# Kernel tuning notes

Hardware: AMD Instinct MI355X
Metric: run time of the kernel (lower is better)

Reference implementation:

```python
import jax, jax.numpy as jnp
import numpy as np

NNK = 16
DENSITY_WEIGHT = 1.0


def _sq_dist(x, y):
    # x: [B, Nx, C], y: [B, Ny, C] -> [B, Nx, Ny] squared L2 distances.
    # Matmul form of the original broadcast-diff computation (same math,
    # avoids materializing [B, Nx, C, Ny]); clamp tiny negatives from fp error.
    x2 = jnp.sum(x * x, axis=-1)               # [B, Nx]
    y2 = jnp.sum(y * y, axis=-1)               # [B, Ny]
    xy = jnp.einsum('bnc,bmc->bnm', x, y)      # [B, Nx, Ny]
    return jnp.maximum(x2[:, :, None] + y2[:, None, :] - 2.0 * xy, 0.0)


def _safe_sqrt(s):
    # sqrt with zero (instead of inf) gradient at s == 0; forward values exact.
    pos = s > 0
    return jnp.where(pos, jnp.sqrt(jnp.where(pos, s, 1.0)), 0.0)


def setup_inputs() -> dict:
    key = jax.random.key(0)
    k1, k2 = jax.random.split(key)
    B, N, C = 2, 8192, 3
    y_pred = jax.random.normal(k1, (B, N, C), dtype=jnp.float32)
    y_true = jax.random.normal(k2, (B, N, C), dtype=jnp.float32)
    return {"y_pred": y_pred, "y_true": y_true}


def reference(y_pred, y_true):
    # dist[b, i, j] = || y_true[b, i] - y_pred[b, j] ||
    dist = _safe_sqrt(_sq_dist(y_true, y_pred))            # [B, Nt, Np]
    minrow = jnp.min(dist, axis=2)                         # per true point
    mincol = jnp.min(dist, axis=1)                         # per pred point
    shape_loss = (jnp.mean(minrow) + jnp.mean(mincol)) / 2

    dist2 = _safe_sqrt(_sq_dist(y_true, y_true))           # [B, Nt, Nt]
    knndis, _ = jax.lax.top_k(-dist, NNK)                  # [B, Nt, k]
    knndis2, _ = jax.lax.top_k(-dist2, NNK)                # [B, Nt, k]
    density_loss = jnp.mean(jnp.abs(knndis - knndis2))

    data_loss = shape_loss + density_loss * DENSITY_WEIGHT
    return (data_loss, shape_loss, density_loss)
```

## Files before the change

kernel.cpp:

```cpp
#include <hip/hip_runtime.h>
#include <math.h>

#define NPTS 8192
#define NB 2
#define NROWS (NB * NPTS)
#define KNN 16
#define KC 6

#define GRID 32
#define NCELLS (GRID * GRID * GRID)
#define TOTCELLS (4 * NCELLS)
#define H 0.35f
#define RLO (-5.6f)
#define INVH (1.0f / H)
#define SCAN_BLOCKS 128
#define SEGCAP 132

__device__ __forceinline__ int cellof(float x) {
  int c = (int)floorf((x - RLO) * INVH);
  return min(max(c, 0), GRID - 1);
}

__device__ __forceinline__ float sqd3(float qx, float qy, float qz, float4 c) {
  float dx = qx - c.x, dy = qy - c.y, dz = qz - c.z;
  return fmaf(dx, dx, fmaf(dy, dy, dz * dz));
}

__device__ __forceinline__ int lanerank(unsigned long long mk) {
  return __builtin_amdgcn_mbcnt_hi((unsigned)(mk >> 32),
                                   __builtin_amdgcn_mbcnt_lo((unsigned)mk, 0));
}

template <int K>
__device__ __forceinline__ void insertK(float (&a)[K], float d) {
  if (d < a[K - 1]) {
    a[K - 1] = d;
#pragma unroll
    for (int k = K - 1; k > 0; --k) {
      float lo = fminf(a[k - 1], a[k]);
      a[k] = fmaxf(a[k - 1], a[k]);
      a[k - 1] = lo;
    }
  }
}

__device__ __forceinline__ float bitonic_sort64(float v, int lane) {
#pragma unroll
  for (int k = 2; k <= 64; k <<= 1) {
#pragma unroll
    for (int j = k >> 1; j >= 1; j >>= 1) {
      float o = __shfl_xor(v, j, 64);
      bool up = ((lane & k) == 0);
      bool lower = ((lane & j) == 0);
      float mn = fminf(v, o), mx = fmaxf(v, o);
      v = (up == lower) ? mn : mx;
    }
  }
  return v;
}

template <int K, int NEED>
__device__ void wave_grid_knn(int g, float qx, float qy, float qz,
                              const float4* __restrict__ sorted,
                              const unsigned* __restrict__ pack,
                              unsigned* sS, unsigned* sC, unsigned* sPre,
                              int lane, float (&a)[K], float& dmin,
                              int& cnt, float& bnd2) {
  const int cx = cellof(qx), cy = cellof(qy), cz = cellof(qz);
  float fx = fminf(qx - (RLO + cx * H), (RLO + (cx + 1) * H) - qx);
  float fy = fminf(qy - (RLO + cy * H), (RLO + (cy + 1) * H) - qy);
  float fz = fminf(qz - (RLO + cz * H), (RLO + (cz + 1) * H) - qz);
  const float fq = fminf(fx, fminf(fy, fz));
  const int base = g * NCELLS;
  for (int m = 0; m <= GRID; ++m) {
    const int zlo = max(cz - m, 0), zhi = min(cz + m, GRID - 1);
    const int ylo = max(cy - m, 0), yhi = min(cy + m, GRID - 1);
    const int xlo = max(cx - m, 0), xhi = min(cx + m, GRID - 1);
    const int ny = yhi - ylo + 1;
    const int nrows = (zhi - zlo + 1) * ny;
    for (int rb = 0; rb < nrows; rb += 64) {
      const int rho = rb + lane;
      const bool act = rho < nrows;
      const int rr = act ? rho : 0;
      const int z = zlo + rr / ny, y = ylo + rr % ny;
      const int dza = abs(z - cz), dya = abs(y - cy);
      const bool bdry = (dza == m) || (dya == m);
      unsigned stA = 0, cnA = 0, stB = 0, cnB = 0;
      const int rowbase = base + (z * GRID + y) * GRID;
      if (act) {
        if (bdry) {
          unsigned plo = pack[rowbase + xlo];
          unsigned phi = pack[rowbase + xhi];
          stA = plo >> 14;
          cnA = ((phi >> 14) + (phi & 16383u)) - stA;
        } else {
          int xl = cx - m, xr = cx + m;
          if (xl >= 0) { unsigned p = pack[rowbase + xl]; stA = p >> 14; cnA = p & 16383u; }
          if (xr < GRID) { unsigned p = pack[rowbase + xr]; stB = p >> 14; cnB = p & 16383u; }
        }
      }
      unsigned long long mA = __ballot(cnA > 0);
      unsigned long long mB = __ballot(cnB > 0);
      int nA = __popcll(mA);
      int nseg = nA + __popcll(mB);
      if (nseg == 0) continue;
      int slA = lanerank(mA), slB = nA + lanerank(mB);
      if (cnA > 0) { sS[slA] = stA; sC[slA] = cnA; }
      if (cnB > 0) { sS[slB] = stB; sC[slB] = cnB; }
      unsigned total = 0;
      for (int h = 0; h < 2; ++h) {
        int sl = h * 64 + lane;
        unsigned v = (sl < nseg) ? sC[sl] : 0u;
        unsigned inc = v;
#pragma unroll
        for (int s2 = 1; s2 < 64; s2 <<= 1) {
          unsigned t = __shfl_up(inc, s2, 64);
          if (lane >= s2) inc += t;
        }
        if (sl < nseg) sPre[sl] = total + inc - v;
        total += __shfl(inc, 63, 64);
        if (nseg <= 64) break;
      }
      int sh0 = (nseg > 1) ? (1 << (31 - __clz(nseg - 1))) : 0;
      for (unsigned cb = 0; cb < total; cb += 64) {
        unsigned c = cb + (unsigned)lane;
        bool cact = c < total;
        unsigned cc = cact ? c : (total - 1);
        int lo = 0;
        for (int sh = sh0; sh; sh >>= 1) {
          int mid = lo + sh;
          if (mid < nseg && sPre[mid] <= cc) lo = mid;
        }
        float4 p = sorted[sS[lo] + (cc - sPre[lo])];
        float d = cact ? sqd3(qx, qy, qz, p) : INFINITY;
        dmin = fminf(dmin, fmaxf(d, a[K - 1]));
        insertK(a, d);
      }
    }
    float bnd = fmaxf((float)m * H + fq, 0.0f) * 0.999f;
    bnd2 = bnd * bnd;
    int c = 0;
#pragma unroll
    for (int k = 0; k < K; ++k) c += (a[k] <= bnd2) ? 1 : 0;
#pragma unroll
    for (int s2 = 1; s2 < 64; s2 <<= 1) c += __shfl_xor(c, s2, 64);
    cnt = c;
    bool covered = (zlo == 0 && zhi == GRID - 1 && ylo == 0 && yhi == GRID - 1 &&
                    xlo == 0 && xhi == GRID - 1);
    if (c >= NEED || covered) break;
  }
}

__global__ __launch_bounds__(256) void count_kernel(
    const float* __restrict__ yp, const float* __restrict__ yt,
    unsigned* __restrict__ counts, int* __restrict__ pflat,
    unsigned* __restrict__ prank) {
  int t = blockIdx.x * 256 + threadIdx.x;
  const float* src;
  int g;
  if (t < NROWS) { src = yp + 3 * t; g = 2 * (t >> 13); }
  else { int u = t - NROWS; src = yt + 3 * u; g = 2 * (u >> 13) + 1; }
  int flat = g * NCELLS + (cellof(src[2]) * GRID + cellof(src[1])) * GRID + cellof(src[0]);
  unsigned r = atomicAdd(&counts[flat], 1u);
  pflat[t] = flat;
  prank[t] = r;
}

__global__ __launch_bounds__(1024) void scan1_kernel(
    const unsigned* __restrict__ counts, unsigned* __restrict__ partial,
    unsigned* __restrict__ aux) {
  __shared__ unsigned s[1024];
  int t = threadIdx.x;
  int base = blockIdx.x * 1024;
  unsigned v = counts[base + t];
  s[t] = v;
  __syncthreads();
  for (int off = 1; off < 1024; off <<= 1) {
    unsigned add = (t >= off) ? s[t - off] : 0u;
    __syncthreads();
    s[t] += add;
    __syncthreads();
  }
  partial[base + t] = s[t] - v;
  if (t == 1023) aux[blockIdx.x] = s[t];
}

__global__ __launch_bounds__(1024) void pack_kernel(
    const unsigned* __restrict__ counts, const unsigned* __restrict__ partial,
    const unsigned* __restrict__ aux, unsigned* __restrict__ pack) {
  __shared__ unsigned sa[2];
  const int t = threadIdx.x;
  if (t < 128) {
    unsigned v = (t < (int)blockIdx.x) ? aux[t] : 0u;
#pragma unroll
    for (int s = 1; s < 64; s <<= 1) v += __shfl_xor(v, s, 64);
    if ((t & 63) == 0) sa[t >> 6] = v;
  }
  __syncthreads();
  unsigned base = sa[0] + sa[1];
  int i = blockIdx.x * 1024 + t;
  pack[i] = ((partial[i] + base) << 14) | counts[i];
}

__global__ __launch_bounds__(256) void scatter_kernel(
    const float* __restrict__ yp, const float* __restrict__ yt,
    const unsigned* __restrict__ pack, const int* __restrict__ pflat,
    const unsigned* __restrict__ prank, float4* __restrict__ sorted) {
  int t = blockIdx.x * 256 + threadIdx.x;
  const float* src;
  int row;
  if (t < NROWS) { row = t; src = yp + 3 * t; }
  else { row = t - NROWS; src = yt + 3 * row; }
  unsigned pos = (pack[pflat[t]] >> 14) + prank[t];
  sorted[pos] = make_float4(src[0], src[1], src[2], __int_as_float(row));
}

__global__ __launch_bounds__(256) void query_kernel(
    const float4* __restrict__ sorted, const unsigned* __restrict__ pack,
    float* __restrict__ knnP, float* __restrict__ knnT,
    float* __restrict__ mincol_arr, unsigned* __restrict__ flags) {
  __shared__ unsigned sb[4][3][SEGCAP];
  __shared__ float cbw[4][64];
  const int wave = threadIdx.x >> 6, lane = threadIdx.x & 63;
  const int wid = blockIdx.x * 4 + wave;
  const int type = wid >> 14;
  const int qid = wid & 16383;
  const int b = qid >> 13;
  const int src_g = (type == 2) ? 2 * b : 2 * b + 1;
  const int tgt_g = (type == 0) ? 2 * b : 2 * b + 1;
  float4 e = sorted[src_g * NPTS + (qid & (NPTS - 1))];
  const int row = __float_as_int(e.w);
  unsigned* sS = sb[wave][0];
  unsigned* sC = sb[wave][1];
  unsigned* sP = sb[wave][2];
  float* cbuf = cbw[wave];
  if (type < 2) {
    float a[KC];
#pragma unroll
    for (int k = 0; k < KC; ++k) a[k] = INFINITY;
    float dmin = INFINITY, bnd2;
    int cnt;
    wave_grid_knn<KC, KNN>(tgt_g, e.x, e.y, e.z, sorted, pack, sS, sC, sP,
                           lane, a, dmin, cnt, bnd2);
    float tau;
    if (cnt >= KNN && cnt <= 64) {
      tau = bnd2;
    } else {
      float slm = bitonic_sort64(a[0], lane);
      tau = __shfl(slm, 15, 64);
    }
    int tot = 0;
    int idx[KC];
#pragma unroll
    for (int k = 0; k < KC; ++k) {
      unsigned long long mk = __ballot(a[k] <= tau);
      idx[k] = tot + lanerank(mk);
      tot += __popcll(mk);
    }
#pragma unroll
    for (int k = 0; k < KC; ++k)
      if (a[k] <= tau && idx[k] < 64) cbuf[idx[k]] = a[k];
    float v = (lane < tot) ? cbuf[lane] : INFINITY;
    v = bitonic_sort64(v, lane);
    float f15 = __shfl(v, 15, 64);
    bool bad = (tot > 64) || (__ballot(dmin <= f15) != 0ull);
    float* dst = (type == 0) ? knnP : knnT;
    if (lane < KNN) dst[row * KNN + lane] = sqrtf(v);
    if (lane == 0) flags[type * NROWS + row] = bad ? 1u : 0u;
  } else {
    float a1[1] = {INFINITY};
    float dmin = INFINITY, bnd2;
    int cnt;
    wave_grid_knn<1, 1>(tgt_g, e.x, e.y, e.z, sorted, pack, sS, sC, sP,
                        lane, a1, dmin, cnt, bnd2);
    float v = a1[0];
#pragma unroll
    for (int s = 1; s < 64; s <<= 1) v = fminf(v, __shfl_xor(v, s, 64));
    if (lane == 0) mincol_arr[row] = sqrtf(v);
  }
}

__device__ float exact16_rowlist(const float4* __restrict__ base,
                                 float qx, float qy, float qz, int lane) {
  float a[KNN];
#pragma unroll
  for (int k = 0; k < KNN; ++k) a[k] = INFINITY;
  for (int s = 0; s < NPTS / 64; ++s) {
    float d = sqd3(qx, qy, qz, base[s * 64 + lane]);
    insertK(a, d);
  }
  float res = INFINITY;
#pragma unroll 1
  for (int r = 0; r < KNN; ++r) {
    float v = a[0];
    int idx = lane;
#pragma unroll
    for (int s = 1; s < 64; s <<= 1) {
      float ov = __shfl_xor(v, s, 64);
      int oi = __shfl_xor(idx, s, 64);
      bool take = (ov < v) || (ov == v && oi < idx);
      v = take ? ov : v;
      idx = take ? oi : idx;
    }
    if (lane == r) res = v;
    if (lane == idx) {
#pragma unroll
      for (int k = 0; k < KNN - 1; ++k) a[k] = a[k + 1];
      a[KNN - 1] = INFINITY;
    }
  }
  return res;
}

__global__ __launch_bounds__(256) void combine_kernel(
    const float* __restrict__ yt, const float4* __restrict__ sorted,
    const unsigned* __restrict__ flags, float* __restrict__ knnP,
    float* __restrict__ knnT, const float* __restrict__ mincol_arr,
    double* __restrict__ pd) {
  __shared__ double s1[256], s2[256], s3[256];
  const int t = threadIdx.x, lane = t & 63, wave = t >> 6;
  const int row0 = blockIdx.x * 256;
  const int rbase = row0 + wave * 64;
  unsigned f0 = flags[rbase + lane];
  unsigned f1 = flags[NROWS + rbase + lane];
  unsigned long long m0 = __ballot(f0 != 0u);
  unsigned long long m1 = __ballot(f1 != 0u);
  while (m0) {
    int rr = __ffsll(m0) - 1; m0 &= m0 - 1;
    int row = rbase + rr;
    int bb = row >> 13;
    const float* q = yt + 3 * row;
    float s = exact16_rowlist(sorted + (size_t)(2 * bb) * NPTS, q[0], q[1], q[2], lane);
    if (lane < KNN) knnP[row * KNN + lane] = sqrtf(s);
  }
  while (m1) {
    int rr = __ffsll(m1) - 1; m1 &= m1 - 1;
    int row = rbase + rr;
    int bb = row >> 13;
    const float* q = yt + 3 * row;
    float s = exact16_rowlist(sorted + (size_t)(2 * bb + 1) * NPTS, q[0], q[1], q[2], lane);
    if (lane < KNN) knnT[row * KNN + lane] = sqrtf(s);
  }
  __syncthreads();
  const int row = row0 + t;
  float s = 0.0f;
#pragma unroll
  for (int k = 0; k < KNN; ++k)
    s += fabsf(knnP[row * KNN + k] - knnT[row * KNN + k]);
  s1[t] = (double)knnP[row * KNN];
  s2[t] = (double)mincol_arr[row];
  s3[t] = (double)s;
  __syncthreads();
  for (int off = 128; off > 0; off >>= 1) {
    if (t < off) { s1[t] += s1[t + off]; s2[t] += s2[t + off]; s3[t] += s3[t + off]; }
    __syncthreads();
  }
  if (t == 0) {
    pd[blockIdx.x * 3 + 0] = s1[0];
    pd[blockIdx.x * 3 + 1] = s2[0];
    pd[blockIdx.x * 3 + 2] = s3[0];
  }
}

__global__ __launch_bounds__(64) void finalize_kernel(
    const double* __restrict__ pd, float* __restrict__ out) {
  const int t = threadIdx.x;
  double a = pd[t * 3], b = pd[t * 3 + 1], c = pd[t * 3 + 2];
#pragma unroll
  for (int s = 32; s >= 1; s >>= 1) {
    a += __shfl_down(a, s, 64);
    b += __shfl_down(b, s, 64);
    c += __shfl_down(c, s, 64);
  }
  if (t == 0) {
    double shape = 0.5 * (a + b) / (double)NROWS;
    double dens = c / ((double)NROWS * KNN);
    out[0] = (float)(shape + dens);
    out[1] = (float)shape;
    out[2] = (float)dens;
  }
}

extern "C" void kernel_launch(void* const* d_in, const int* in_sizes, int n_in,
                              void* d_out, int out_size, void* d_ws, size_t ws_size,
                              hipStream_t stream) {
  (void)in_sizes; (void)n_in; (void)out_size; (void)ws_size;
  const float* yp = (const float*)d_in[0];
  const float* yt = (const float*)d_in[1];
  char* w = (char*)d_ws;
  unsigned* counts  = (unsigned*)w;  w += TOTCELLS * 4;
  unsigned* partial = (unsigned*)w;  w += TOTCELLS * 4;
  unsigned* aux     = (unsigned*)w;  w += 512;
  unsigned* pack    = (unsigned*)w;  w += TOTCELLS * 4;
  int*      pflat   = (int*)w;       w += 2 * NROWS * 4;
  unsigned* prank   = (unsigned*)w;  w += 2 * NROWS * 4;
  float4*   sorted  = (float4*)w;    w += 2 * NROWS * 16;
  float*    knnP    = (float*)w;     w += NROWS * KNN * 4;
  float*    knnT    = (float*)w;     w += NROWS * KNN * 4;
  float*    mincol  = (float*)w;     w += NROWS * 4;
  unsigned* flags   = (unsigned*)w;  w += 2 * NROWS * 4;
  double*   pd      = (double*)w;    w += 64 * 3 * 8;
  float* out = (float*)d_out;

  hipMemsetAsync(counts, 0, (size_t)TOTCELLS * 4, stream);
  count_kernel<<<2 * NROWS / 256, 256, 0, stream>>>(yp, yt, counts, pflat, prank);
  scan1_kernel<<<SCAN_BLOCKS, 1024, 0, stream>>>(counts, partial, aux);
  pack_kernel<<<SCAN_BLOCKS, 1024, 0, stream>>>(counts, partial, aux, pack);
  scatter_kernel<<<2 * NROWS / 256, 256, 0, stream>>>(yp, yt, pack, pflat, prank, sorted);
  query_kernel<<<3 * 16384 / 4, 256, 0, stream>>>(sorted, pack, knnP, knnT, mincol, flags);
  combine_kernel<<<64, 256, 0, stream>>>(yt, sorted, flags, knnP, knnT, mincol, pd);
  finalize_kernel<<<1, 64, 0, stream>>>(pd, out);
}
```

Measured before the change: 137.4 us.

## Fuse grid-build stages into one cooperative kernel with grid syncs

Replaces the memset, count, scan, pack and scatter kernels with a single cooperative kernel of 128 blocks of 1024 threads that uses grid.sync between phases. Point coordinates, cell index and rank stay in registers, so the pflat/prank scratch arrays and their global round trips go away, along with four launch boundaries. The cost is grid-wide barriers and a cooperative launch, and the whole build runs on only 128 blocks.

```diff
diff --git a/kernel.cpp b/kernel.cpp
--- a/kernel.cpp
+++ b/kernel.cpp
@@ -1,5 +1,8 @@
 #include <hip/hip_runtime.h>
+#include <hip/hip_cooperative_groups.h>
 #include <math.h>
+
+namespace cg = cooperative_groups;
 
 #define NPTS 8192
 #define NB 2
@@ -151,28 +154,36 @@
   }
 }
 
-__global__ __launch_bounds__(256) void count_kernel(
+__global__ __launch_bounds__(1024) void build_kernel(
     const float* __restrict__ yp, const float* __restrict__ yt,
-    unsigned* __restrict__ counts, int* __restrict__ pflat,
-    unsigned* __restrict__ prank) {
-  int t = blockIdx.x * 256 + threadIdx.x;
-  const float* src;
-  int g;
-  if (t < NROWS) { src = yp + 3 * t; g = 2 * (t >> 13); }
-  else { int u = t - NROWS; src = yt + 3 * u; g = 2 * (u >> 13) + 1; }
-  int flat = g * NCELLS + (cellof(src[2]) * GRID + cellof(src[1])) * GRID + cellof(src[0]);
-  unsigned r = atomicAdd(&counts[flat], 1u);
-  pflat[t] = flat;
-  prank[t] = r;
-}
-
-__global__ __launch_bounds__(1024) void scan1_kernel(
-    const unsigned* __restrict__ counts, unsigned* __restrict__ partial,
-    unsigned* __restrict__ aux) {
+    unsigned* __restrict__ counts, unsigned* __restrict__ partial,
+    unsigned* __restrict__ aux, unsigned* __restrict__ pack,
+    float4* __restrict__ sorted) {
+  cg::grid_group grid = cg::this_grid();
   __shared__ unsigned s[1024];
-  int t = threadIdx.x;
-  int base = blockIdx.x * 1024;
-  unsigned v = counts[base + t];
+  __shared__ unsigned sa[2];
+  const int t = threadIdx.x;
+  const int tid = blockIdx.x * 1024 + t;
+
+  counts[tid] = 0u;
+  grid.sync();
+
+  float x = 0.f, y = 0.f, z = 0.f;
+  int flat = 0, row = 0;
+  unsigned rank = 0;
+  const bool haspt = tid < 2 * NROWS;
+  if (haspt) {
+    const float* src;
+    int g;
+    if (tid < NROWS) { row = tid; src = yp + 3 * tid; g = 2 * (tid >> 13); }
+    else { row = tid - NROWS; src = yt + 3 * row; g = 2 * (row >> 13) + 1; }
+    x = src[0]; y = src[1]; z = src[2];
+    flat = g * NCELLS + (cellof(z) * GRID + cellof(y)) * GRID + cellof(x);
+    rank = atomicAdd(&counts[flat], 1u);
+  }
+  grid.sync();
+
+  unsigned v = counts[tid];
   s[t] = v;
   __syncthreads();
   for (int off = 1; off < 1024; off <<= 1) {
@@ -181,38 +192,25 @@
     s[t] += add;
     __syncthreads();
   }
-  partial[base + t] = s[t] - v;
+  partial[tid] = s[t] - v;
   if (t == 1023) aux[blockIdx.x] = s[t];
-}
-
-__global__ __launch_bounds__(1024) void pack_kernel(
-    const unsigned* __restrict__ counts, const unsigned* __restrict__ partial,
-    const unsigned* __restrict__ aux, unsigned* __restrict__ pack) {
-  __shared__ unsigned sa[2];
-  const int t = threadIdx.x;
+  grid.sync();
+
   if (t < 128) {
-    unsigned v = (t < (int)blockIdx.x) ? aux[t] : 0u;
-#pragma unroll
-    for (int s = 1; s < 64; s <<= 1) v += __shfl_xor(v, s, 64);
-    if ((t & 63) == 0) sa[t >> 6] = v;
+    unsigned av = (t < (int)blockIdx.x) ? aux[t] : 0u;
+#pragma unroll
+    for (int s2 = 1; s2 < 64; s2 <<= 1) av += __shfl_xor(av, s2, 64);
+    if ((t & 63) == 0) sa[t >> 6] = av;
   }
   __syncthreads();
   unsigned base = sa[0] + sa[1];
-  int i = blockIdx.x * 1024 + t;
-  pack[i] = ((partial[i] + base) << 14) | counts[i];
-}
-
-__global__ __launch_bounds__(256) void scatter_kernel(
-    const float* __restrict__ yp, const float* __restrict__ yt,
-    const unsigned* __restrict__ pack, const int* __restrict__ pflat,
-    const unsigned* __restrict__ prank, float4* __restrict__ sorted) {
-  int t = blockIdx.x * 256 + threadIdx.x;
-  const float* src;
-  int row;
-  if (t < NROWS) { row = t; src = yp + 3 * t; }
-  else { row = t - NROWS; src = yt + 3 * row; }
-  unsigned pos = (pack[pflat[t]] >> 14) + prank[t];
-  sorted[pos] = make_float4(src[0], src[1], src[2], __int_as_float(row));
+  pack[tid] = ((partial[tid] + base) << 14) | counts[tid];
+  grid.sync();
+
+  if (haspt) {
+    unsigned pos = (pack[flat] >> 14) + rank;
+    sorted[pos] = make_float4(x, y, z, __int_as_float(row));
+  }
 }
 
 __global__ __launch_bounds__(256) void query_kernel(
@@ -392,8 +390,6 @@
   unsigned* partial = (unsigned*)w;  w += TOTCELLS * 4;
   unsigned* aux     = (unsigned*)w;  w += 512;
   unsigned* pack    = (unsigned*)w;  w += TOTCELLS * 4;
-  int*      pflat   = (int*)w;       w += 2 * NROWS * 4;
-  unsigned* prank   = (unsigned*)w;  w += 2 * NROWS * 4;
   float4*   sorted  = (float4*)w;    w += 2 * NROWS * 16;
   float*    knnP    = (float*)w;     w += NROWS * KNN * 4;
   float*    knnT    = (float*)w;     w += NROWS * KNN * 4;
@@ -402,11 +398,10 @@
   double*   pd      = (double*)w;    w += 64 * 3 * 8;
   float* out = (float*)d_out;
 
-  hipMemsetAsync(counts, 0, (size_t)TOTCELLS * 4, stream);
-  count_kernel<<<2 * NROWS / 256, 256, 0, stream>>>(yp, yt, counts, pflat, prank);
-  scan1_kernel<<<SCAN_BLOCKS, 1024, 0, stream>>>(counts, partial, aux);
-  pack_kernel<<<SCAN_BLOCKS, 1024, 0, stream>>>(counts, partial, aux, pack);
-  scatter_kernel<<<2 * NROWS / 256, 256, 0, stream>>>(yp, yt, pack, pflat, prank, sorted);
+  void* bargs[] = {(void*)&yp, (void*)&yt, (void*)&counts, (void*)&partial,
+                   (void*)&aux, (void*)&pack, (void*)&sorted};
+  hipLaunchCooperativeKernel((void*)build_kernel, dim3(SCAN_BLOCKS), dim3(1024),
+                             bargs, 0, stream);
   query_kernel<<<3 * 16384 / 4, 256, 0, stream>>>(sorted, pack, knnP, knnT, mincol, flags);
   combine_kernel<<<64, 256, 0, stream>>>(yt, sorted, flags, knnP, knnT, mincol, pd);
   finalize_kernel<<<1, 64, 0, stream>>>(pd, out);
```

Result: slower. 211.2 us (+53.7%).

## Fold pack into scatter and finalize into combine via atomic ticket

Applied to the files above, without the earlier changes.

Removes two kernel launches. The pack kernel's work moves into the scatter kernel, where each thread builds four pack entries and sums the aux block prefix serially. Scatter positions now come straight from partial plus the aux prefix instead of from pack. The final reduction now runs inside combine_kernel: the last block to arrive, found with an atomic ticket counter zeroed by the extended memset, does the sum. The cost is a serial loop of up to 128 aux reads per thread and a threadfence/atomic handshake.

```diff
diff --git a/kernel.cpp b/kernel.cpp
--- a/kernel.cpp
+++ b/kernel.cpp
@@ -185,33 +185,31 @@
   if (t == 1023) aux[blockIdx.x] = s[t];
 }
 
-__global__ __launch_bounds__(1024) void pack_kernel(
-    const unsigned* __restrict__ counts, const unsigned* __restrict__ partial,
-    const unsigned* __restrict__ aux, unsigned* __restrict__ pack) {
-  __shared__ unsigned sa[2];
-  const int t = threadIdx.x;
-  if (t < 128) {
-    unsigned v = (t < (int)blockIdx.x) ? aux[t] : 0u;
-#pragma unroll
-    for (int s = 1; s < 64; s <<= 1) v += __shfl_xor(v, s, 64);
-    if ((t & 63) == 0) sa[t >> 6] = v;
-  }
-  __syncthreads();
-  unsigned base = sa[0] + sa[1];
-  int i = blockIdx.x * 1024 + t;
-  pack[i] = ((partial[i] + base) << 14) | counts[i];
-}
-
 __global__ __launch_bounds__(256) void scatter_kernel(
     const float* __restrict__ yp, const float* __restrict__ yt,
-    const unsigned* __restrict__ pack, const int* __restrict__ pflat,
-    const unsigned* __restrict__ prank, float4* __restrict__ sorted) {
+    const unsigned* __restrict__ counts, const unsigned* __restrict__ partial,
+    const unsigned* __restrict__ aux, const int* __restrict__ pflat,
+    const unsigned* __restrict__ prank, unsigned* __restrict__ pack,
+    float4* __restrict__ sorted) {
   int t = blockIdx.x * 256 + threadIdx.x;
+  int c0 = t * 4;
+  int ab = c0 >> 10;
+  unsigned apre = 0;
+  for (int i = 0; i < ab; ++i) apre += aux[i];
+#pragma unroll
+  for (int j = 0; j < 4; ++j) {
+    int c = c0 + j;
+    pack[c] = ((partial[c] + apre) << 14) | counts[c];
+  }
   const float* src;
   int row;
   if (t < NROWS) { row = t; src = yp + 3 * t; }
   else { row = t - NROWS; src = yt + 3 * row; }
-  unsigned pos = (pack[pflat[t]] >> 14) + prank[t];
+  int flat = pflat[t];
+  int fb = flat >> 10;
+  unsigned fpre = 0;
+  for (int i = 0; i < fb; ++i) fpre += aux[i];
+  unsigned pos = partial[flat] + fpre + prank[t];
   sorted[pos] = make_float4(src[0], src[1], src[2], __int_as_float(row));
 }
 
@@ -316,8 +314,10 @@
     const float* __restrict__ yt, const float4* __restrict__ sorted,
     const unsigned* __restrict__ flags, float* __restrict__ knnP,
     float* __restrict__ knnT, const float* __restrict__ mincol_arr,
-    double* __restrict__ pd) {
+    double* __restrict__ pd, unsigned* __restrict__ ticket,
+    float* __restrict__ out) {
   __shared__ double s1[256], s2[256], s3[256];
+  __shared__ unsigned oldv;
   const int t = threadIdx.x, lane = t & 63, wave = t >> 6;
   const int row0 = blockIdx.x * 256;
   const int rbase = row0 + wave * 64;
@@ -360,24 +360,28 @@
     pd[blockIdx.x * 3 + 1] = s2[0];
     pd[blockIdx.x * 3 + 2] = s3[0];
   }
-}
-
-__global__ __launch_bounds__(64) void finalize_kernel(
-    const double* __restrict__ pd, float* __restrict__ out) {
-  const int t = threadIdx.x;
-  double a = pd[t * 3], b = pd[t * 3 + 1], c = pd[t * 3 + 2];
-#pragma unroll
-  for (int s = 32; s >= 1; s >>= 1) {
-    a += __shfl_down(a, s, 64);
-    b += __shfl_down(b, s, 64);
-    c += __shfl_down(c, s, 64);
-  }
-  if (t == 0) {
-    double shape = 0.5 * (a + b) / (double)NROWS;
-    double dens = c / ((double)NROWS * KNN);
-    out[0] = (float)(shape + dens);
-    out[1] = (float)shape;
-    out[2] = (float)dens;
+  __threadfence();
+  if (t == 0) oldv = atomicAdd(ticket, 1u);
+  __syncthreads();
+  if (oldv == 63) {
+    __threadfence();
+    if (t < 64) {
+      const volatile double* vpd = (const volatile double*)pd;
+      double a = vpd[t * 3], b = vpd[t * 3 + 1], c = vpd[t * 3 + 2];
+#pragma unroll
+      for (int s2 = 32; s2 >= 1; s2 >>= 1) {
+        a += __shfl_down(a, s2, 64);
+        b += __shfl_down(b, s2, 64);
+        c += __shfl_down(c, s2, 64);
+      }
+      if (t == 0) {
+        double shape = 0.5 * (a + b) / (double)NROWS;
+        double dens = c / ((double)NROWS * KNN);
+        out[0] = (float)(shape + dens);
+        out[1] = (float)shape;
+        out[2] = (float)dens;
+      }
+    }
   }
 }
 
@@ -389,6 +393,7 @@
   const float* yt = (const float*)d_in[1];
   char* w = (char*)d_ws;
   unsigned* counts  = (unsigned*)w;  w += TOTCELLS * 4;
+  unsigned* ticket  = (unsigned*)w;  w += 64;
   unsigned* partial = (unsigned*)w;  w += TOTCELLS * 4;
   unsigned* aux     = (unsigned*)w;  w += 512;
   unsigned* pack    = (unsigned*)w;  w += TOTCELLS * 4;
@@ -402,12 +407,12 @@
   double*   pd      = (double*)w;    w += 64 * 3 * 8;
   float* out = (float*)d_out;
 
-  hipMemsetAsync(counts, 0, (size_t)TOTCELLS * 4, stream);
+  hipMemsetAsync(counts, 0, (size_t)TOTCELLS * 4 + 64, stream);
   count_kernel<<<2 * NROWS / 256, 256, 0, stream>>>(yp, yt, counts, pflat, prank);
   scan1_kernel<<<SCAN_BLOCKS, 1024, 0, stream>>>(counts, partial, aux);
-  pack_kernel<<<SCAN_BLOCKS, 1024, 0, stream>>>(counts, partial, aux, pack);
-  scatter_kernel<<<2 * NROWS / 256, 256, 0, stream>>>(yp, yt, pack, pflat, prank, sorted);
+  scatter_kernel<<<2 * NROWS / 256, 256, 0, stream>>>(yp, yt, counts, partial, aux,
+                                                      pflat, prank, pack, sorted);
   query_kernel<<<3 * 16384 / 4, 256, 0, stream>>>(sorted, pack, knnP, knnT, mincol, flags);
-  combine_kernel<<<64, 256, 0, stream>>>(yt, sorted, flags, knnP, knnT, mincol, pd);
-  finalize_kernel<<<1, 64, 0, stream>>>(pd, out);
-}
+  combine_kernel<<<64, 256, 0, stream>>>(yt, sorted, flags, knnP, knnT, mincol,
+                                         pd, ticket, out);
+}
```

New measurement: 144.7 us. 5.3% more time.
